# Kernel optimization log

Hardware: AMD Instinct MI355X
Metric: run time of the kernel (lower is better)

Reference implementation:

```python
import jax, jax.numpy as jnp
import numpy as np

N_NODES = 50000
N_EDGES = 800000


def setup_inputs() -> dict:
    key = jax.random.key(0)
    ks = jax.random.split(key, 6)
    x = jax.random.normal(ks[0], (N_NODES, 128), dtype=jnp.float32)
    edge_index = jax.random.randint(ks[1], (2, N_EDGES), 0, N_NODES, dtype=jnp.int64)
    # Glorot-ish scaled weights (PyG GCNConv uses glorot init)
    W1 = jax.random.normal(ks[2], (128, 256), dtype=jnp.float32) * (1.0 / np.sqrt(128))
    b1 = jnp.zeros((256,), dtype=jnp.float32)
    W2 = jax.random.normal(ks[3], (256, 128), dtype=jnp.float32) * (1.0 / np.sqrt(256))
    b2 = jnp.zeros((128,), dtype=jnp.float32)
    Wfc = jax.random.normal(ks[4], (128, 1), dtype=jnp.float32) * (1.0 / np.sqrt(128))
    bfc = jnp.zeros((1,), dtype=jnp.float32)
    return {"x": x, "edge_index": edge_index, "W1": W1, "b1": b1,
            "W2": W2, "b2": b2, "Wfc": Wfc, "bfc": bfc}


def _gcn_conv(x, src, dst, inv_sqrt_deg, W, b, n_nodes):
    # x: [N, Fin]; src/dst: [E+N] (self-loops included); W: [Fin, Fout]
    h = x @ W                                   # dense per-node transform
    norm = inv_sqrt_deg[src] * inv_sqrt_deg[dst]  # [E+N] symmetric normalization
    msg = h[src] * norm[:, None]                # gather + scale
    out = jax.ops.segment_sum(msg, dst, num_segments=n_nodes)  # scatter-add
    return out + b


def reference(x, edge_index, W1, b1, W2, b2, Wfc, bfc):
    n_nodes = x.shape[0]
    loops = jnp.arange(n_nodes, dtype=edge_index.dtype)
    src = jnp.concatenate([edge_index[0], loops])  # add self-loops (PyG default)
    dst = jnp.concatenate([edge_index[1], loops])
    deg = jax.ops.segment_sum(jnp.ones_like(dst, dtype=x.dtype), dst,
                              num_segments=n_nodes)  # in-degree incl. self-loop
    inv_sqrt_deg = jax.lax.rsqrt(deg)               # deg >= 1 due to self-loops

    h = jax.nn.relu(_gcn_conv(x, src, dst, inv_sqrt_deg, W1, b1, n_nodes))
    h = jax.nn.relu(_gcn_conv(h, src, dst, inv_sqrt_deg, W2, b2, n_nodes))
    pooled = jnp.mean(h, axis=0)                    # [output_dim]
    return pooled @ Wfc + bfc                       # [1]
```

## Files before the change

### kernel.cpp

```cpp
#include <hip/hip_runtime.h>


#define FEAT 128
#define TILE 4096
#define BSH  9
#define BKN  512

typedef __attribute__((ext_vector_type(8))) short short8;
typedef __attribute__((ext_vector_type(4))) float float4v;
typedef __attribute__((ext_vector_type(2))) float floatx2;

__device__ __forceinline__ unsigned int f2b(float f) {
    unsigned int u = __float_as_uint(f);
    return (u + 0x7fffu + ((u >> 16) & 1u)) >> 16;
}


__global__ __launch_bounds__(1024) void k_p1(const int* __restrict__ dst,
                                             int* __restrict__ cnt, int E, int B, int NW) {
    __shared__ int h[128];
    int t = threadIdx.x, w = blockIdx.x;
    if (t < B) h[t] = 0;
    __syncthreads();
    int e0 = w * TILE, e1 = min(e0 + TILE, E);
    for (int e = e0 + t; e < e1; e += 1024) atomicAdd(&h[dst[e] >> BSH], 1);
    __syncthreads();
    if (t < B) cnt[t * NW + w] = h[t];
}

__global__ __launch_bounds__(1024) void k_scanA(int* __restrict__ cnt,
                                                int* __restrict__ tot, int L) {
    __shared__ int s[1024];
    int t = threadIdx.x, g = blockIdx.x;
    int i = g * 1024 + t;
    int x = (i < L) ? cnt[i] : 0;
    s[t] = x;
    __syncthreads();
    for (int d = 1; d < 1024; d <<= 1) {
        int y = (t >= d) ? s[t - d] : 0;
        __syncthreads();
        s[t] += y;
        __syncthreads();
    }
    if (i < L) cnt[i] = s[t] - x;
    if (t == 1023) tot[g] = s[t];
}

__global__ void k_scanB(int* __restrict__ tot, int G) {
    __shared__ int s[64];
    int t = threadIdx.x;
    s[t] = (t < G) ? tot[t] : 0;
    __syncthreads();
    if (t == 0) {
        int run = 0;
        for (int g = 0; g < G; ++g) { int x = s[g]; s[g] = run; run += x; }
    }
    __syncthreads();
    if (t < G) tot[t] = s[t];
}

__global__ __launch_bounds__(1024) void k_p3(const int* __restrict__ src,
                                             const int* __restrict__ dst,
                                             const int* __restrict__ cnt,
                                             const int* __restrict__ tbase,
                                             unsigned int* __restrict__ ebuf,
                                             int E, int B, int NW) {
    __shared__ int cur[128];
    int t = threadIdx.x, w = blockIdx.x;
    if (t < B) { int i = t * NW + w; cur[t] = cnt[i] + tbase[i >> 10]; }
    __syncthreads();
    int e0 = w * TILE, e1 = min(e0 + TILE, E);
    for (int e = e0 + t; e < e1; e += 1024) {
        int d = dst[e], s = src[e];
        int p = atomicAdd(&cur[d >> BSH], 1);
        ebuf[p] = ((unsigned int)d << 16) | (unsigned int)s;
    }
}

__global__ __launch_bounds__(1024) void k_p4(const unsigned int* __restrict__ ebuf,
                                             const int* __restrict__ cnt,
                                             const int* __restrict__ tbase,
                                             float* __restrict__ isd,
                                             int* __restrict__ off,
                                             unsigned short* __restrict__ csr,
                                             int E, int B, int NW, int N) {
    __shared__ int h[BKN];
    __shared__ int s[BKN];
    __shared__ int cur[BKN];
    int t = threadIdx.x, b = blockIdx.x;
    if (t < BKN) h[t] = 0;
    __syncthreads();
    int i0 = b * NW;
    int s0 = cnt[i0] + tbase[i0 >> 10];
    int s1 = E;
    if (b + 1 < B) { int i1 = (b + 1) * NW; s1 = cnt[i1] + tbase[i1 >> 10]; }
    for (int e = s0 + t; e < s1; e += 1024)
        atomicAdd(&h[(ebuf[e] >> 16) & (BKN - 1)], 1);
    __syncthreads();
    int own = (t < BKN) ? h[t] : 0;
    if (t < BKN) s[t] = own;
    __syncthreads();
    for (int d = 1; d < BKN; d <<= 1) {
        int x = (t >= d && t < BKN) ? s[t - d] : 0;
        __syncthreads();
        if (t < BKN) s[t] += x;
        __syncthreads();
    }
    if (t < BKN) {
        int node = (b << BSH) + t;
        int myoff = s0 + s[t] - own;
        cur[t] = myoff;
        if (node < N) {
            isd[node] = rsqrtf((float)(own + 1));
            off[node] = myoff;
            if (node == N - 1) off[N] = s0 + s[t];
        }
    }
    __syncthreads();
    for (int e = s0 + t; e < s1; e += 1024) {
        unsigned int v = ebuf[e];
        int p = atomicAdd(&cur[(v >> 16) & (BKN - 1)], 1);
        csr[p] = (unsigned short)(v & 0xffffu);
    }
}


__device__ __forceinline__ void wswz_one(const float* W, unsigned short* out,
                                         int N, int tid) {
    int lane = tid & 63, f = tid >> 6;
    int NT = N >> 4;
    int nt = f % NT, kt = f / NT;
    int m = lane & 15, quad = lane >> 4;
    short8 pk;
#pragma unroll
    for (int j = 0; j < 8; ++j)
        pk[j] = (short)f2b(W[(size_t)(kt * 32 + quad * 8 + j) * N + nt * 16 + m]);
    *(short8*)(out + (size_t)tid * 8) = pk;
}

__global__ void k_prep(const float* __restrict__ x, const float* __restrict__ isd,
                       unsigned int* __restrict__ xq, float* __restrict__ pooled,
                       const float* __restrict__ W1, unsigned short* __restrict__ w1z,
                       const float* __restrict__ W2, unsigned short* __restrict__ w2z,
                       int total4) {
    int i = blockIdx.x * blockDim.x + threadIdx.x;
    if (i < 8192) pooled[i] = 0.f;
    if (i < 4096) wswz_one(W1, w1z, 256, i);
    else if (i < 8192) wswz_one(W2, w2z, 128, i - 4096);
    if (i >= total4) return;
    float w = isd[i >> 5] * 16.f;
    float4 v = ((const float4*)x)[i];
    unsigned int u = __builtin_amdgcn_cvt_pk_fp8_f32(v.x * w, v.y * w, 0u, false);
    u = __builtin_amdgcn_cvt_pk_fp8_f32(v.z * w, v.w * w, u, true);
    xq[i] = u;
}


__device__ __forceinline__ void gather_row(const unsigned short* __restrict__ Xq,
                                           const int* __restrict__ off,
                                           const unsigned short* __restrict__ csr,
                                           int wid, int lane, float& ra0, float& ra1) {
    int beg = off[wid], end = off[wid + 1];
    float a0, a1;
    {
        unsigned int q = Xq[(size_t)wid * 64 + lane];
        floatx2 f = __builtin_amdgcn_cvt_pk_f32_fp8(q, false);
        a0 = f[0]; a1 = f[1];
    }
    int e = beg;
    for (; e + 8 <= end; e += 8) {
        int s0 = csr[e],     s1 = csr[e + 1], s2 = csr[e + 2], s3 = csr[e + 3];
        int s4 = csr[e + 4], s5 = csr[e + 5], s6 = csr[e + 6], s7 = csr[e + 7];
        unsigned int q0 = Xq[(size_t)s0 * 64 + lane];
        unsigned int q1 = Xq[(size_t)s1 * 64 + lane];
        unsigned int q2 = Xq[(size_t)s2 * 64 + lane];
        unsigned int q3 = Xq[(size_t)s3 * 64 + lane];
        unsigned int q4 = Xq[(size_t)s4 * 64 + lane];
        unsigned int q5 = Xq[(size_t)s5 * 64 + lane];
        unsigned int q6 = Xq[(size_t)s6 * 64 + lane];
        unsigned int q7 = Xq[(size_t)s7 * 64 + lane];
        floatx2 f0 = __builtin_amdgcn_cvt_pk_f32_fp8(q0, false);
        floatx2 f1 = __builtin_amdgcn_cvt_pk_f32_fp8(q1, false);
        floatx2 f2 = __builtin_amdgcn_cvt_pk_f32_fp8(q2, false);
        floatx2 f3 = __builtin_amdgcn_cvt_pk_f32_fp8(q3, false);
        floatx2 f4 = __builtin_amdgcn_cvt_pk_f32_fp8(q4, false);
        floatx2 f5 = __builtin_amdgcn_cvt_pk_f32_fp8(q5, false);
        floatx2 f6 = __builtin_amdgcn_cvt_pk_f32_fp8(q6, false);
        floatx2 f7 = __builtin_amdgcn_cvt_pk_f32_fp8(q7, false);
        a0 += f0[0] + f1[0] + f2[0] + f3[0] + f4[0] + f5[0] + f6[0] + f7[0];
        a1 += f0[1] + f1[1] + f2[1] + f3[1] + f4[1] + f5[1] + f6[1] + f7[1];
    }
    for (; e + 2 <= end; e += 2) {
        int s0 = csr[e], s1 = csr[e + 1];
        unsigned int q0 = Xq[(size_t)s0 * 64 + lane];
        unsigned int q1 = Xq[(size_t)s1 * 64 + lane];
        floatx2 f0 = __builtin_amdgcn_cvt_pk_f32_fp8(q0, false);
        floatx2 f1 = __builtin_amdgcn_cvt_pk_f32_fp8(q1, false);
        a0 += f0[0] + f1[0];
        a1 += f0[1] + f1[1];
    }
    if (e < end) {
        unsigned int q0 = Xq[(size_t)csr[e] * 64 + lane];
        floatx2 f0 = __builtin_amdgcn_cvt_pk_f32_fp8(q0, false);
        a0 += f0[0];
        a1 += f0[1];
    }
    ra0 = a0; ra1 = a1;
}

__device__ __forceinline__ void gather_row2(const unsigned short* __restrict__ Xq,
                                            const int* __restrict__ off,
                                            const unsigned short* __restrict__ csr,
                                            int r0, int r1, int lane,
                                            float& oa0, float& oa1,
                                            float& ob0, float& ob1) {
    int beg0 = off[r0], end0 = off[r0 + 1], end1 = off[r1 + 1];
    int beg1 = end0;
    float a0, a1, b0, b1;
    {
        unsigned int q = Xq[(size_t)r0 * 64 + lane];
        unsigned int p = Xq[(size_t)r1 * 64 + lane];
        floatx2 f = __builtin_amdgcn_cvt_pk_f32_fp8(q, false);
        floatx2 g = __builtin_amdgcn_cvt_pk_f32_fp8(p, false);
        a0 = f[0]; a1 = f[1]; b0 = g[0]; b1 = g[1];
    }
    int e0 = beg0, e1 = beg1;
    while (e0 + 4 <= end0 && e1 + 4 <= end1) {
        int s00 = csr[e0], s01 = csr[e0 + 1], s02 = csr[e0 + 2], s03 = csr[e0 + 3];
        int s10 = csr[e1], s11 = csr[e1 + 1], s12 = csr[e1 + 2], s13 = csr[e1 + 3];
        unsigned int q00 = Xq[(size_t)s00 * 64 + lane];
        unsigned int q10 = Xq[(size_t)s10 * 64 + lane];
        unsigned int q01 = Xq[(size_t)s01 * 64 + lane];
        unsigned int q11 = Xq[(size_t)s11 * 64 + lane];
        unsigned int q02 = Xq[(size_t)s02 * 64 + lane];
        unsigned int q12 = Xq[(size_t)s12 * 64 + lane];
        unsigned int q03 = Xq[(size_t)s03 * 64 + lane];
        unsigned int q13 = Xq[(size_t)s13 * 64 + lane];
        floatx2 f0 = __builtin_amdgcn_cvt_pk_f32_fp8(q00, false);
        floatx2 f1 = __builtin_amdgcn_cvt_pk_f32_fp8(q01, false);
        floatx2 f2 = __builtin_amdgcn_cvt_pk_f32_fp8(q02, false);
        floatx2 f3 = __builtin_amdgcn_cvt_pk_f32_fp8(q03, false);
        floatx2 g0 = __builtin_amdgcn_cvt_pk_f32_fp8(q10, false);
        floatx2 g1 = __builtin_amdgcn_cvt_pk_f32_fp8(q11, false);
        floatx2 g2 = __builtin_amdgcn_cvt_pk_f32_fp8(q12, false);
        floatx2 g3 = __builtin_amdgcn_cvt_pk_f32_fp8(q13, false);
        a0 += f0[0] + f1[0] + f2[0] + f3[0];
        a1 += f0[1] + f1[1] + f2[1] + f3[1];
        b0 += g0[0] + g1[0] + g2[0] + g3[0];
        b1 += g0[1] + g1[1] + g2[1] + g3[1];
        e0 += 4; e1 += 4;
    }
    for (; e0 + 4 <= end0; e0 += 4) {
        int s0 = csr[e0], s1 = csr[e0 + 1], s2 = csr[e0 + 2], s3 = csr[e0 + 3];
        unsigned int q0 = Xq[(size_t)s0 * 64 + lane];
        unsigned int q1 = Xq[(size_t)s1 * 64 + lane];
        unsigned int q2 = Xq[(size_t)s2 * 64 + lane];
        unsigned int q3 = Xq[(size_t)s3 * 64 + lane];
        floatx2 f0 = __builtin_amdgcn_cvt_pk_f32_fp8(q0, false);
        floatx2 f1 = __builtin_amdgcn_cvt_pk_f32_fp8(q1, false);
        floatx2 f2 = __builtin_amdgcn_cvt_pk_f32_fp8(q2, false);
        floatx2 f3 = __builtin_amdgcn_cvt_pk_f32_fp8(q3, false);
        a0 += f0[0] + f1[0] + f2[0] + f3[0];
        a1 += f0[1] + f1[1] + f2[1] + f3[1];
    }
    for (; e0 + 2 <= end0; e0 += 2) {
        int s0 = csr[e0], s1 = csr[e0 + 1];
        unsigned int q0 = Xq[(size_t)s0 * 64 + lane];
        unsigned int q1 = Xq[(size_t)s1 * 64 + lane];
        floatx2 f0 = __builtin_amdgcn_cvt_pk_f32_fp8(q0, false);
        floatx2 f1 = __builtin_amdgcn_cvt_pk_f32_fp8(q1, false);
        a0 += f0[0] + f1[0];
        a1 += f0[1] + f1[1];
    }
    if (e0 < end0) {
        unsigned int q0 = Xq[(size_t)csr[e0] * 64 + lane];
        floatx2 f0 = __builtin_amdgcn_cvt_pk_f32_fp8(q0, false);
        a0 += f0[0]; a1 += f0[1];
    }
    for (; e1 + 4 <= end1; e1 += 4) {
        int s0 = csr[e1], s1 = csr[e1 + 1], s2 = csr[e1 + 2], s3 = csr[e1 + 3];
        unsigned int q0 = Xq[(size_t)s0 * 64 + lane];
        unsigned int q1 = Xq[(size_t)s1 * 64 + lane];
        unsigned int q2 = Xq[(size_t)s2 * 64 + lane];
        unsigned int q3 = Xq[(size_t)s3 * 64 + lane];
        floatx2 g0 = __builtin_amdgcn_cvt_pk_f32_fp8(q0, false);
        floatx2 g1 = __builtin_amdgcn_cvt_pk_f32_fp8(q1, false);
        floatx2 g2 = __builtin_amdgcn_cvt_pk_f32_fp8(q2, false);
        floatx2 g3 = __builtin_amdgcn_cvt_pk_f32_fp8(q3, false);
        b0 += g0[0] + g1[0] + g2[0] + g3[0];
        b1 += g0[1] + g1[1] + g2[1] + g3[1];
    }
    for (; e1 + 2 <= end1; e1 += 2) {
        int s0 = csr[e1], s1 = csr[e1 + 1];
        unsigned int q0 = Xq[(size_t)s0 * 64 + lane];
        unsigned int q1 = Xq[(size_t)s1 * 64 + lane];
        floatx2 g0 = __builtin_amdgcn_cvt_pk_f32_fp8(q0, false);
        floatx2 g1 = __builtin_amdgcn_cvt_pk_f32_fp8(q1, false);
        b0 += g0[0] + g1[0];
        b1 += g0[1] + g1[1];
    }
    if (e1 < end1) {
        unsigned int q0 = Xq[(size_t)csr[e1] * 64 + lane];
        floatx2 g0 = __builtin_amdgcn_cvt_pk_f32_fp8(q0, false);
        b0 += g0[0]; b1 += g0[1];
    }
    oa0 = a0; oa1 = a1; ob0 = b0; ob1 = b1;
}


__global__ __launch_bounds__(256) void k_agg1(const unsigned short* __restrict__ Xq,
                                              const int* __restrict__ off,
                                              const unsigned short* __restrict__ csr,
                                              const float* __restrict__ isd,
                                              unsigned int* __restrict__ out, int n) {
    int g    = (blockIdx.x * 256 + threadIdx.x) >> 6;
    int lane = threadIdx.x & 63;
    int r0 = g * 2;
    if (r0 >= n) return;
    r0 = __builtin_amdgcn_readfirstlane(r0);
    int r1 = r0 + 1;
    if (r1 < n) {
        float a0, a1, b0, b1;
        gather_row2(Xq, off, csr, r0, r1, lane, a0, a1, b0, b1);
        float w0 = isd[r0] * 0.0625f;
        float w1 = isd[r1] * 0.0625f;
        out[(size_t)r0 * 64 + lane] = f2b(w0 * a0) | (f2b(w0 * a1) << 16);
        out[(size_t)r1 * 64 + lane] = f2b(w1 * b0) | (f2b(w1 * b1) << 16);
    } else {
        float a0, a1;
        gather_row(Xq, off, csr, r0, lane, a0, a1);
        float w0 = isd[r0] * 0.0625f;
        out[(size_t)r0 * 64 + lane] = f2b(w0 * a0) | (f2b(w0 * a1) << 16);
    }
}


__global__ __launch_bounds__(256) void k_gemm12(const unsigned short* __restrict__ A,
                                                const unsigned short* __restrict__ W1z,
                                                const float* __restrict__ b1,
                                                const unsigned short* __restrict__ W2z,
                                                const float* __restrict__ isd,
                                                unsigned char* __restrict__ t2q, int M) {
    __shared__ unsigned short h1s[64 * 272];
    int tid = threadIdx.x;
    int lane = tid & 63, wm = tid >> 6;
    int m = lane & 15, quad = lane >> 4;

    long arow = (long)blockIdx.x * 64 + wm * 16 + m;
    if (arow >= M) arow = M - 1;
    const short8* Ap  = (const short8*)(A + (size_t)arow * 128);
    const short8* W1p = (const short8*)W1z + lane;

    float4v acc1[16];
    float4v zero = {0.f, 0.f, 0.f, 0.f};
#pragma unroll
    for (int nt = 0; nt < 16; ++nt) acc1[nt] = zero;
#pragma unroll
    for (int kt = 0; kt < 4; ++kt) {
        short8 a = Ap[kt * 4 + quad];
#pragma unroll
        for (int nt = 0; nt < 16; ++nt)
            acc1[nt] = __builtin_amdgcn_mfma_f32_16x16x32_bf16(a, W1p[(kt * 16 + nt) * 64],
                                                               acc1[nt], 0, 0, 0);
    }
    int r0 = wm * 16 + quad * 4;
#pragma unroll
    for (int nt = 0; nt < 16; ++nt) {
        int col = nt * 16 + m;
        float bz = b1[col];
#pragma unroll
        for (int reg = 0; reg < 4; ++reg) {
            float v = fmaxf(acc1[nt][reg] + bz, 0.f);
            h1s[(r0 + reg) * 272 + col] = (unsigned short)f2b(v);
        }
    }
    __syncthreads();

    float4v acc2[8];
#pragma unroll
    for (int nt = 0; nt < 8; ++nt) acc2[nt] = zero;
    const short8* W2p = (const short8*)W2z + lane;
    int rloc = wm * 16 + m;
#pragma unroll
    for (int kt = 0; kt < 8; ++kt) {
        short8 a2 = *(const short8*)(h1s + rloc * 272 + kt * 32 + quad * 8);
#pragma unroll
        for (int nt = 0; nt < 8; ++nt)
            acc2[nt] = __builtin_amdgcn_mfma_f32_16x16x32_bf16(a2, W2p[(kt * 8 + nt) * 64],
                                                               acc2[nt], 0, 0, 0);
    }
    int gr0 = blockIdx.x * 64 + wm * 16 + quad * 4;
    float sc[4];
#pragma unroll
    for (int reg = 0; reg < 4; ++reg) {
        int r = gr0 + reg;
        sc[reg] = ((r < M) ? isd[r] : 0.f) * 16.f;
    }
#pragma unroll
    for (int nt = 0; nt < 8; ++nt) {
        int col = nt * 16 + m;
#pragma unroll
        for (int reg = 0; reg < 4; ++reg) {
            int gr = gr0 + reg;
            if (gr < M) {
                float v = acc2[nt][reg] * sc[reg];
                unsigned int b = __builtin_amdgcn_cvt_pk_fp8_f32(v, v, 0u, false);
                t2q[(size_t)gr * 128 + col] = (unsigned char)(b & 0xffu);
            }
        }
    }
}


__global__ __launch_bounds__(256) void k_agg2p(const unsigned short* __restrict__ Xq,
                                               const int* __restrict__ off,
                                               const unsigned short* __restrict__ csr,
                                               const float* __restrict__ isd,
                                               const float* __restrict__ b2,
                                               float* __restrict__ pooled, int n) {
    __shared__ float s0[256], s1[256];
    int tid = threadIdx.x;
    int g    = (blockIdx.x * 256 + tid) >> 6;
    int lane = tid & 63;
    float c0 = 0.f, c1 = 0.f;
    int r0 = g * 2;
    if (r0 < n) {
        int ru = __builtin_amdgcn_readfirstlane(r0);
        int r1 = ru + 1;
        float bz0 = b2[2 * lane], bz1 = b2[2 * lane + 1];
        if (r1 < n) {
            float a0, a1, b0v, b1v;
            gather_row2(Xq, off, csr, ru, r1, lane, a0, a1, b0v, b1v);
            float w0 = isd[ru] * 0.0625f;
            float w1 = isd[r1] * 0.0625f;
            c0 = fmaxf(w0 * a0 + bz0, 0.f) + fmaxf(w1 * b0v + bz0, 0.f);
            c1 = fmaxf(w0 * a1 + bz1, 0.f) + fmaxf(w1 * b1v + bz1, 0.f);
        } else {
            float a0, a1;
            gather_row(Xq, off, csr, ru, lane, a0, a1);
            float w0 = isd[ru] * 0.0625f;
            c0 = fmaxf(w0 * a0 + bz0, 0.f);
            c1 = fmaxf(w0 * a1 + bz1, 0.f);
        }
    }
    s0[tid] = c0;
    s1[tid] = c1;
    __syncthreads();
    if (tid < 64) {
        float t0 = s0[tid] + s0[tid + 64] + s0[tid + 128] + s0[tid + 192];
        float t1 = s1[tid] + s1[tid + 64] + s1[tid + 128] + s1[tid + 192];
        float* dst = pooled + (blockIdx.x & 63) * 128;
        atomicAdd(&dst[2 * tid], t0);
        atomicAdd(&dst[2 * tid + 1], t1);
    }
}


__global__ void k_final(const float* __restrict__ pooled,
                        const float* __restrict__ Wfc,
                        const float* __restrict__ bfc,
                        float* __restrict__ out, float invN) {
    __shared__ float s[128];
    int t = threadIdx.x;
    float v = 0.f;
#pragma unroll
    for (int r = 0; r < 64; ++r) v += pooled[r * 128 + t];
    s[t] = v * invN * Wfc[t];
    __syncthreads();
    for (int d = 64; d > 0; d >>= 1) {
        if (t < d) s[t] += s[t + d];
        __syncthreads();
    }
    if (t == 0) out[0] = s[0] + bfc[0];
}


extern "C" void kernel_launch(void* const* d_in, const int* in_sizes, int n_in,
                              void* d_out, int out_size, void* d_ws, size_t ws_size,
                              hipStream_t stream) {
    const float* x   = (const float*)d_in[0];
    const int*   ei  = (const int*)d_in[1];
    const float* W1  = (const float*)d_in[2];
    const float* b1  = (const float*)d_in[3];
    const float* W2  = (const float*)d_in[4];
    const float* b2  = (const float*)d_in[5];
    const float* Wfc = (const float*)d_in[6];
    const float* bfc = (const float*)d_in[7];
    float* out = (float*)d_out;

    int N = in_sizes[0] / FEAT;
    int E = in_sizes[1] / 2;
    const int* src = ei;
    const int* dst = ei + E;

    int NW = (E + TILE - 1) / TILE;
    int B  = (N + BKN - 1) >> BSH;
    int L  = B * NW;
    int G  = (L + 1023) / 1024;

    char* p = (char*)d_ws;
    auto alloc = [&](size_t bytes) {
        char* r = p;
        p += (bytes + 255) & ~(size_t)255;
        return r;
    };
    int* cnt             = (int*)alloc((size_t)L * 4);
    int* tot             = (int*)alloc(64 * 4);
    unsigned int* ebuf   = (unsigned int*)alloc((size_t)E * 4);
    unsigned short* csr  = (unsigned short*)alloc((size_t)E * 2);
    float* isd           = (float*)alloc((size_t)N * 4);
    int* off             = (int*)alloc((size_t)(N + 1) * 4);
    unsigned int* xq     = (unsigned int*)alloc((size_t)N * 32 * 4);
    unsigned int* agg1b  = (unsigned int*)alloc((size_t)N * 64 * 4);
    unsigned char* t2q   = (unsigned char*)alloc((size_t)N * 128);
    unsigned short* w1z  = (unsigned short*)alloc(128 * 256 * 2);
    unsigned short* w2z  = (unsigned short*)alloc(256 * 128 * 2);
    float* pooled        = (float*)alloc(64 * 128 * 4);

    k_p1<<<NW, 1024, 0, stream>>>(dst, cnt, E, B, NW);
    k_scanA<<<G, 1024, 0, stream>>>(cnt, tot, L);
    k_scanB<<<1, 64, 0, stream>>>(tot, G);
    k_p3<<<NW, 1024, 0, stream>>>(src, dst, cnt, tot, ebuf, E, B, NW);
    k_p4<<<B, 1024, 0, stream>>>(ebuf, cnt, tot, isd, off, csr, E, B, NW, N);

    int total4 = N * FEAT / 4;
    k_prep<<<(total4 + 255) / 256, 256, 0, stream>>>(x, isd, xq, pooled,
                                                     W1, w1z, W2, w2z, total4);

    int gblk  = (N + 63) / 64;
    int npair = (N + 1) / 2;
    int nblk2 = (npair + 3) / 4;

    k_agg1<<<nblk2, 256, 0, stream>>>((const unsigned short*)xq, off, csr, isd, agg1b, N);
    k_gemm12<<<gblk, 256, 0, stream>>>((const unsigned short*)agg1b, w1z, b1, w2z, isd, t2q, N);

    k_agg2p<<<nblk2, 256, 0, stream>>>((const unsigned short*)t2q, off, csr, isd, b2,
                                       pooled, N);
    k_final<<<1, 128, 0, stream>>>(pooled, Wfc, bfc, out, 1.0f / (float)N);
}
```

Measured before the change: 193.4 us.

## Fuse CSR build and input prep into one cooperative kernel with grid syncs

Merges the six preprocessing kernels (histogram, two-level scan, bucket scatter, per-bucket sort, and fp8 quantization/weight swizzle) into a single cooperative kernel of NW blocks, replacing the kernel boundaries with grid.sync. The goal is to cut launch overhead and inter-kernel gaps for these small phases. In exchange, all NW (~196) blocks of 1024 threads must be co-resident, and the quantization phase now runs on far fewer threads with a grid-stride loop. Grid-wide barriers also carry their own cost.

```diff
diff --git a/kernel.cpp b/kernel.cpp
--- a/kernel.cpp
+++ b/kernel.cpp
@@ -1,4 +1,7 @@
 #include <hip/hip_runtime.h>
+#include <hip/hip_cooperative_groups.h>
+
+namespace cg = cooperative_groups;
 
 
 #define FEAT 128
@@ -13,115 +16,6 @@
 __device__ __forceinline__ unsigned int f2b(float f) {
     unsigned int u = __float_as_uint(f);
     return (u + 0x7fffu + ((u >> 16) & 1u)) >> 16;
-}
-
-
-__global__ __launch_bounds__(1024) void k_p1(const int* __restrict__ dst,
-                                             int* __restrict__ cnt, int E, int B, int NW) {
-    __shared__ int h[128];
-    int t = threadIdx.x, w = blockIdx.x;
-    if (t < B) h[t] = 0;
-    __syncthreads();
-    int e0 = w * TILE, e1 = min(e0 + TILE, E);
-    for (int e = e0 + t; e < e1; e += 1024) atomicAdd(&h[dst[e] >> BSH], 1);
-    __syncthreads();
-    if (t < B) cnt[t * NW + w] = h[t];
-}
-
-__global__ __launch_bounds__(1024) void k_scanA(int* __restrict__ cnt,
-                                                int* __restrict__ tot, int L) {
-    __shared__ int s[1024];
-    int t = threadIdx.x, g = blockIdx.x;
-    int i = g * 1024 + t;
-    int x = (i < L) ? cnt[i] : 0;
-    s[t] = x;
-    __syncthreads();
-    for (int d = 1; d < 1024; d <<= 1) {
-        int y = (t >= d) ? s[t - d] : 0;
-        __syncthreads();
-        s[t] += y;
-        __syncthreads();
-    }
-    if (i < L) cnt[i] = s[t] - x;
-    if (t == 1023) tot[g] = s[t];
-}
-
-__global__ void k_scanB(int* __restrict__ tot, int G) {
-    __shared__ int s[64];
-    int t = threadIdx.x;
-    s[t] = (t < G) ? tot[t] : 0;
-    __syncthreads();
-    if (t == 0) {
-        int run = 0;
-        for (int g = 0; g < G; ++g) { int x = s[g]; s[g] = run; run += x; }
-    }
-    __syncthreads();
-    if (t < G) tot[t] = s[t];
-}
-
-__global__ __launch_bounds__(1024) void k_p3(const int* __restrict__ src,
-                                             const int* __restrict__ dst,
-                                             const int* __restrict__ cnt,
-                                             const int* __restrict__ tbase,
-                                             unsigned int* __restrict__ ebuf,
-                                             int E, int B, int NW) {
-    __shared__ int cur[128];
-    int t = threadIdx.x, w = blockIdx.x;
-    if (t < B) { int i = t * NW + w; cur[t] = cnt[i] + tbase[i >> 10]; }
-    __syncthreads();
-    int e0 = w * TILE, e1 = min(e0 + TILE, E);
-    for (int e = e0 + t; e < e1; e += 1024) {
-        int d = dst[e], s = src[e];
-        int p = atomicAdd(&cur[d >> BSH], 1);
-        ebuf[p] = ((unsigned int)d << 16) | (unsigned int)s;
-    }
-}
-
-__global__ __launch_bounds__(1024) void k_p4(const unsigned int* __restrict__ ebuf,
-                                             const int* __restrict__ cnt,
-                                             const int* __restrict__ tbase,
-                                             float* __restrict__ isd,
-                                             int* __restrict__ off,
-                                             unsigned short* __restrict__ csr,
-                                             int E, int B, int NW, int N) {
-    __shared__ int h[BKN];
-    __shared__ int s[BKN];
-    __shared__ int cur[BKN];
-    int t = threadIdx.x, b = blockIdx.x;
-    if (t < BKN) h[t] = 0;
-    __syncthreads();
-    int i0 = b * NW;
-    int s0 = cnt[i0] + tbase[i0 >> 10];
-    int s1 = E;
-    if (b + 1 < B) { int i1 = (b + 1) * NW; s1 = cnt[i1] + tbase[i1 >> 10]; }
-    for (int e = s0 + t; e < s1; e += 1024)
-        atomicAdd(&h[(ebuf[e] >> 16) & (BKN - 1)], 1);
-    __syncthreads();
-    int own = (t < BKN) ? h[t] : 0;
-    if (t < BKN) s[t] = own;
-    __syncthreads();
-    for (int d = 1; d < BKN; d <<= 1) {
-        int x = (t >= d && t < BKN) ? s[t - d] : 0;
-        __syncthreads();
-        if (t < BKN) s[t] += x;
-        __syncthreads();
-    }
-    if (t < BKN) {
-        int node = (b << BSH) + t;
-        int myoff = s0 + s[t] - own;
-        cur[t] = myoff;
-        if (node < N) {
-            isd[node] = rsqrtf((float)(own + 1));
-            off[node] = myoff;
-            if (node == N - 1) off[N] = s0 + s[t];
-        }
-    }
-    __syncthreads();
-    for (int e = s0 + t; e < s1; e += 1024) {
-        unsigned int v = ebuf[e];
-        int p = atomicAdd(&cur[(v >> 16) & (BKN - 1)], 1);
-        csr[p] = (unsigned short)(v & 0xffffu);
-    }
 }
 
 
@@ -138,21 +32,128 @@
     *(short8*)(out + (size_t)tid * 8) = pk;
 }
 
-__global__ void k_prep(const float* __restrict__ x, const float* __restrict__ isd,
-                       unsigned int* __restrict__ xq, float* __restrict__ pooled,
-                       const float* __restrict__ W1, unsigned short* __restrict__ w1z,
-                       const float* __restrict__ W2, unsigned short* __restrict__ w2z,
-                       int total4) {
-    int i = blockIdx.x * blockDim.x + threadIdx.x;
-    if (i < 8192) pooled[i] = 0.f;
-    if (i < 4096) wswz_one(W1, w1z, 256, i);
-    else if (i < 8192) wswz_one(W2, w2z, 128, i - 4096);
-    if (i >= total4) return;
-    float w = isd[i >> 5] * 16.f;
-    float4 v = ((const float4*)x)[i];
-    unsigned int u = __builtin_amdgcn_cvt_pk_fp8_f32(v.x * w, v.y * w, 0u, false);
-    u = __builtin_amdgcn_cvt_pk_fp8_f32(v.z * w, v.w * w, u, true);
-    xq[i] = u;
+
+__global__ __launch_bounds__(1024) void k_build(const int* __restrict__ src,
+                                                const int* __restrict__ dst,
+                                                const float* __restrict__ x,
+                                                const float* __restrict__ W1,
+                                                const float* __restrict__ W2,
+                                                int* __restrict__ cnt,
+                                                int* __restrict__ tot,
+                                                unsigned int* __restrict__ ebuf,
+                                                unsigned short* __restrict__ csr,
+                                                float* __restrict__ isd,
+                                                int* __restrict__ off,
+                                                unsigned int* __restrict__ xq,
+                                                float* __restrict__ pooled,
+                                                unsigned short* __restrict__ w1z,
+                                                unsigned short* __restrict__ w2z,
+                                                int E, int N, int B, int NW,
+                                                int L, int G, int total4) {
+    cg::grid_group grid = cg::this_grid();
+    __shared__ int smem[3 * BKN];
+    int t = threadIdx.x, w = blockIdx.x;
+
+    {
+        int* h = smem;
+        if (t < B) h[t] = 0;
+        __syncthreads();
+        int gt = w * 1024 + t;
+        if (gt < 4096) wswz_one(W1, w1z, 256, gt);
+        else if (gt < 8192) wswz_one(W2, w2z, 128, gt - 4096);
+        if (gt < 8192) pooled[gt] = 0.f;
+        int e0 = w * TILE, e1 = min(e0 + TILE, E);
+        for (int e = e0 + t; e < e1; e += 1024) atomicAdd(&h[dst[e] >> BSH], 1);
+        __syncthreads();
+        if (t < B) cnt[t * NW + w] = h[t];
+    }
+    grid.sync();
+
+    if (w < G) {
+        int* s = smem;
+        int i = w * 1024 + t;
+        int xv = (i < L) ? cnt[i] : 0;
+        s[t] = xv;
+        __syncthreads();
+        for (int d = 1; d < 1024; d <<= 1) {
+            int y = (t >= d) ? s[t - d] : 0;
+            __syncthreads();
+            s[t] += y;
+            __syncthreads();
+        }
+        if (i < L) cnt[i] = s[t] - xv;
+        if (t == 1023) tot[w] = s[t];
+    }
+    grid.sync();
+
+    if (w == 0 && t == 0) {
+        int run = 0;
+        for (int g = 0; g < G; ++g) { int xv = tot[g]; tot[g] = run; run += xv; }
+    }
+    grid.sync();
+
+    {
+        int* cur = smem;
+        if (t < B) { int i = t * NW + w; cur[t] = cnt[i] + tot[i >> 10]; }
+        __syncthreads();
+        int e0 = w * TILE, e1 = min(e0 + TILE, E);
+        for (int e = e0 + t; e < e1; e += 1024) {
+            int d = dst[e], s = src[e];
+            int p = atomicAdd(&cur[d >> BSH], 1);
+            ebuf[p] = ((unsigned int)d << 16) | (unsigned int)s;
+        }
+        __syncthreads();
+    }
+    grid.sync();
+
+    if (w < B) {
+        int* h   = smem;
+        int* s   = smem + BKN;
+        int* cur = smem + 2 * BKN;
+        if (t < BKN) h[t] = 0;
+        __syncthreads();
+        int i0 = w * NW;
+        int s0 = cnt[i0] + tot[i0 >> 10];
+        int s1 = E;
+        if (w + 1 < B) { int i1 = (w + 1) * NW; s1 = cnt[i1] + tot[i1 >> 10]; }
+        for (int e = s0 + t; e < s1; e += 1024)
+            atomicAdd(&h[(ebuf[e] >> 16) & (BKN - 1)], 1);
+        __syncthreads();
+        int own = (t < BKN) ? h[t] : 0;
+        if (t < BKN) s[t] = own;
+        __syncthreads();
+        for (int d = 1; d < BKN; d <<= 1) {
+            int xv = (t >= d && t < BKN) ? s[t - d] : 0;
+            __syncthreads();
+            if (t < BKN) s[t] += xv;
+            __syncthreads();
+        }
+        if (t < BKN) {
+            int node = (w << BSH) + t;
+            int myoff = s0 + s[t] - own;
+            cur[t] = myoff;
+            if (node < N) {
+                isd[node] = rsqrtf((float)(own + 1));
+                off[node] = myoff;
+                if (node == N - 1) off[N] = s0 + s[t];
+            }
+        }
+        __syncthreads();
+        for (int e = s0 + t; e < s1; e += 1024) {
+            unsigned int v = ebuf[e];
+            int p = atomicAdd(&cur[(v >> 16) & (BKN - 1)], 1);
+            csr[p] = (unsigned short)(v & 0xffffu);
+        }
+    }
+    grid.sync();
+
+    for (int i = w * 1024 + t; i < total4; i += NW * 1024) {
+        float wsc = isd[i >> 5] * 16.f;
+        float4 v = ((const float4*)x)[i];
+        unsigned int u = __builtin_amdgcn_cvt_pk_fp8_f32(v.x * wsc, v.y * wsc, 0u, false);
+        u = __builtin_amdgcn_cvt_pk_fp8_f32(v.z * wsc, v.w * wsc, u, true);
+        xq[i] = u;
+    }
 }
 
 
@@ -497,6 +498,7 @@
     int B  = (N + BKN - 1) >> BSH;
     int L  = B * NW;
     int G  = (L + 1023) / 1024;
+    int total4 = N * FEAT / 4;
 
     char* p = (char*)d_ws;
     auto alloc = [&](size_t bytes) {
@@ -517,15 +519,14 @@
     unsigned short* w2z  = (unsigned short*)alloc(256 * 128 * 2);
     float* pooled        = (float*)alloc(64 * 128 * 4);
 
-    k_p1<<<NW, 1024, 0, stream>>>(dst, cnt, E, B, NW);
-    k_scanA<<<G, 1024, 0, stream>>>(cnt, tot, L);
-    k_scanB<<<1, 64, 0, stream>>>(tot, G);
-    k_p3<<<NW, 1024, 0, stream>>>(src, dst, cnt, tot, ebuf, E, B, NW);
-    k_p4<<<B, 1024, 0, stream>>>(ebuf, cnt, tot, isd, off, csr, E, B, NW, N);
-
-    int total4 = N * FEAT / 4;
-    k_prep<<<(total4 + 255) / 256, 256, 0, stream>>>(x, isd, xq, pooled,
-                                                     W1, w1z, W2, w2z, total4);
+    void* args[] = {(void*)&src, (void*)&dst, (void*)&x, (void*)&W1, (void*)&W2,
+                    (void*)&cnt, (void*)&tot, (void*)&ebuf, (void*)&csr,
+                    (void*)&isd, (void*)&off, (void*)&xq, (void*)&pooled,
+                    (void*)&w1z, (void*)&w2z,
+                    (void*)&E, (void*)&N, (void*)&B, (void*)&NW,
+                    (void*)&L, (void*)&G, (void*)&total4};
+    hipLaunchCooperativeKernel((const void*)k_build, dim3(NW), dim3(1024),
+                               args, 0, stream);
 
     int gblk  = (N + 63) / 64;
     int npair = (N + 1) / 2;
```

Measured after the change: 319.3 us. 1.65x slower.
